# Kernel tuning notes

Hardware: AMD Instinct MI355X
Metric: run time of the kernel (lower is better)

Reference implementation:

```python
import jax, jax.numpy as jnp
import numpy as np


def setup_inputs() -> dict:
    key = jax.random.key(0)
    k1, k2 = jax.random.split(key)
    B, C, H, W = 16, 256, 128, 128
    x = jax.random.normal(k1, (B, C, H, W), dtype=jnp.float32)
    mask = jax.random.uniform(k2, (B, 1, H, W), dtype=jnp.float32)
    return {"x": x, "k": 4096, "mask": mask}


def reference(x, k, mask):
    # Faithful jax version of PointSampler.samplePoints2D:
    #   flatten spatial dims, per-batch random permutation of masked positions,
    #   repeat-to-fill k samples, gather, return (samples [B,k,C], (b, h, w) indices).
    B, C, H, W = x.shape
    L = H * W
    xf = x.reshape(B, C, L).transpose(0, 2, 1)            # [B, L, C]
    m = mask.reshape(B, L) > 0.5                           # bool mask per row
    count = m.sum(axis=1)                                  # [B], number of valid positions

    # Random permutation of masked positions per row: masked entries get random
    # keys, unmasked get +inf, argsort puts masked positions first in random order.
    rkey = jax.random.key(42)
    r = jax.random.uniform(rkey, (B, L))
    r = jnp.where(m, r, jnp.inf)
    perm = jnp.argsort(r, axis=1)                          # [B, L]

    # randperm(c).repeat(ceil(k/c))[:k]  ==  perm[j % c] for j in range(k)
    j = jnp.arange(k)                                      # [k]
    pos = jnp.take_along_axis(perm, j[None, :] % count[:, None], axis=1)  # [B, k] flat positions

    samples = jnp.take_along_axis(xf, pos[:, :, None], axis=1)  # [B, k, C]

    b_idx = jnp.broadcast_to(jnp.arange(B)[:, None], (B, k))
    h_idx = pos // W
    w_idx = pos % W
    return samples, (b_idx, h_idx, w_idx)
```

## Files before the change

kernel.cpp:

```cpp
#include <hip/hip_runtime.h>
#include <stdint.h>


#define L_SPATIAL 16384
#define BATCHES 16
#define CHANNELS 256
#define KSAMP 4096
#define HALF_COUNT 131072u
#define CAP 96
#define INVALID 0xFFFFFFFFu
#define POSB 32

__device__ __forceinline__ uint32_t rotl32(uint32_t x, int d) {
  return (x << d) | (x >> (32 - d));
}

__device__ __forceinline__ void tf2x32(uint32_t k0, uint32_t k1,
                                       uint32_t x0, uint32_t x1,
                                       uint32_t* o0, uint32_t* o1) {
  uint32_t ks2 = k0 ^ k1 ^ 0x1BD11BDAu;
  x0 += k0; x1 += k1;
#define TFR(r) { x0 += x1; x1 = rotl32(x1, r); x1 ^= x0; }
  TFR(13) TFR(15) TFR(26) TFR(6)
  x0 += k1;  x1 += ks2 + 1u;
  TFR(17) TFR(29) TFR(16) TFR(24)
  x0 += ks2; x1 += k0 + 2u;
  TFR(13) TFR(15) TFR(26) TFR(6)
  x0 += k0;  x1 += k1 + 3u;
  TFR(17) TFR(29) TFR(16) TFR(24)
  x0 += k1;  x1 += ks2 + 4u;
  TFR(13) TFR(15) TFR(26) TFR(6)
  x0 += ks2; x1 += k0 + 5u;
#undef TFR
  *o0 = x0; *o1 = x1;
}

__device__ __forceinline__ float bits_to_uniform(uint32_t bits) {
  return __uint_as_float((bits >> 9) | 0x3F800000u) - 1.0f;
}

__device__ __forceinline__ uint32_t r_bits(uint32_t f, unsigned partitionable) {
  uint32_t o0, o1;
  if (partitionable) {
    tf2x32(0u, 42u, 0u, f, &o0, &o1);
    return o0 ^ o1;
  } else {
    uint32_t p = f & (HALF_COUNT - 1u);
    tf2x32(0u, 42u, p, p + HALF_COUNT, &o0, &o1);
    return (f & HALF_COUNT) ? o1 : o0;
  }
}

__global__ void init_detect(const float* __restrict__ mask,
                            unsigned* __restrict__ sel,
                            unsigned* __restrict__ bcnt,
                            unsigned* __restrict__ flag) {
  unsigned i = blockIdx.x * 256u + threadIdx.x;
  if (i < 8192u) sel[i] = 0u;
  else bcnt[i - 8192u] = 0u;
  if (blockIdx.x == 0) {
    int t = threadIdx.x;
    __shared__ int vo, vp;
    if (t == 0) { vo = 0; vp = 0; }
    __syncthreads();
    if (t < 64) {
      uint32_t a0, a1, b0, b1, c0, c1, w0, w1;
      tf2x32(0u, 0u, 0u, 2u, &a0, &a1);
      tf2x32(0u, 0u, 1u, 3u, &b0, &b1);
      uint32_t ko0 = a1, ko1 = b1;
      tf2x32(0u, 0u, 0u, 1u, &c0, &c1);
      uint32_t kp0 = c0, kp1 = c1;
      tf2x32(ko0, ko1, (uint32_t)t, (uint32_t)t + HALF_COUNT, &w0, &w1);
      float mo = bits_to_uniform(w0);
      tf2x32(kp0, kp1, 0u, (uint32_t)t, &w0, &w1);
      float mp = bits_to_uniform(w0 ^ w1);
      float actual = mask[t];
      if (mo == actual) atomicAdd(&vo, 1);
      if (mp == actual) atomicAdd(&vp, 1);
    }
    __syncthreads();
    if (t == 0) *flag = (vp >= vo) ? 1u : 0u;
  }
}

__global__ void build_bucket(const float* __restrict__ mask,
                             unsigned long long* __restrict__ bkeys,
                             unsigned* __restrict__ bcnt,
                             const unsigned* __restrict__ flag) {
  unsigned f = blockIdx.x * 256u + threadIdx.x;
  unsigned part = *flag;
  if (mask[f] > 0.5f) {
    unsigned b = f >> 14, l = f & 16383u;
    uint32_t mant = r_bits(f, part) >> 9;
    unsigned bkt = mant >> 15;
    unsigned slot = atomicAdd(&bcnt[(b << 8) + bkt], 1u);
    if (slot < CAP)
      bkeys[(size_t)((b << 8) + bkt) * CAP + slot] =
          ((unsigned long long)mant << 14) | l;
  }
}

__global__ void prefix_buckets(const unsigned* __restrict__ bcnt,
                               unsigned* __restrict__ bpref,
                               unsigned* __restrict__ counts) {
  int b = blockIdx.x, t = threadIdx.x;
  __shared__ unsigned s[256];
  unsigned v = bcnt[(b << 8) + t];
  s[t] = v;
  __syncthreads();
  for (int d = 1; d < 256; d <<= 1) {
    unsigned u = (t >= d) ? s[t - d] : 0u;
    __syncthreads();
    s[t] += u;
    __syncthreads();
  }
  bpref[(b << 8) + t] = s[t] - v;
  if (t == 255) counts[b] = s[255];
}

__global__ __launch_bounds__(64) void rank_buckets(
    const unsigned long long* __restrict__ bkeys,
    const unsigned* __restrict__ bcnt,
    const unsigned* __restrict__ bpref,
    unsigned* __restrict__ flagrank,
    unsigned* __restrict__ sel) {
  unsigned B = blockIdx.x, b = blockIdx.y;
  unsigned base = bpref[(b << 8) + B];
  if (base >= KSAMP) return;
  unsigned n = bcnt[(b << 8) + B];
  if (n > CAP) n = CAP;
  if (n == 0) return;
  __shared__ unsigned long long sk[CAP];
  const unsigned long long* gk = bkeys + (size_t)((b << 8) + B) * CAP;
  for (unsigned i = threadIdx.x; i < n; i += 64) sk[i] = gk[i];
  __syncthreads();
  for (unsigned i = threadIdx.x; i < n; i += 64) {
    unsigned long long ki = sk[i];
    unsigned r = 0;
    for (unsigned j = 0; j < n; ++j) r += (sk[j] < ki);
    unsigned rank = base + r;
    if (rank < KSAMP) {
      unsigned l = (unsigned)(ki & 16383ull);
      flagrank[(b << 14) + l] = rank;
      atomicOr(&sel[(b << 9) + (l >> 5)], 1u << (l & 31u));
    }
  }
}

__global__ void compact_pairs(const unsigned* __restrict__ flagrank,
                              const unsigned* __restrict__ sel,
                              unsigned* __restrict__ pairs) {
  int b = blockIdx.x, t = threadIdx.x;
  unsigned w0 = sel[(b << 9) + 2 * t];
  unsigned w1 = sel[(b << 9) + 2 * t + 1];
  unsigned c = __popc(w0) + __popc(w1);
  __shared__ unsigned s[256];
  s[t] = c;
  __syncthreads();
  for (int d = 1; d < 256; d <<= 1) {
    unsigned u = (t >= d) ? s[t - d] : 0u;
    __syncthreads();
    s[t] += u;
    __syncthreads();
  }
  unsigned off = s[t] - c;
  unsigned lbase = (unsigned)t * 64u;
  const unsigned* fr = flagrank + (b << 14);
  unsigned* pb = pairs + (b << 12);
  while (w0) {
    unsigned bit = (unsigned)__ffs(w0) - 1u; w0 &= w0 - 1u;
    unsigned l = lbase + bit;
    pb[off++] = (fr[l] << 14) | l;
  }
  while (w1) {
    unsigned bit = (unsigned)__ffs(w1) - 1u; w1 &= w1 - 1u;
    unsigned l = lbase + 32u + bit;
    pb[off++] = (fr[l] << 14) | l;
  }
}

__global__ __launch_bounds__(256, 4) void gather_out(
    const float* __restrict__ x,
    const unsigned* __restrict__ pairs,
    const unsigned* __restrict__ counts,
    float* __restrict__ out) {
  unsigned idx = blockIdx.x;
  unsigned xcd = idx & 7u, slot = idx >> 3;
  unsigned b = (xcd << 1) | (slot >> 7);
  unsigned ib = slot & 127u;
  unsigned count = counts[b];
  unsigned n_sel = count < KSAMP ? count : KSAMP;
  unsigned i0 = ib * POSB;
  if (i0 >= n_sel) return;
  unsigned nb = n_sel - i0; if (nb > POSB) nb = POSB;

  __shared__ float tile[CHANNELS][POSB + 1];
  __shared__ unsigned sl[POSB], sr[POSB];
  int t = threadIdx.x;
  if (t < POSB && (unsigned)t < nb) {
    unsigned pr = pairs[(b << 12) + i0 + (unsigned)t];
    sl[t] = pr & 16383u;
    sr[t] = pr >> 14;
  }
  __syncthreads();

  unsigned pos = (unsigned)t & 31u, ch = (unsigned)t >> 5;
  if (pos < nb) {
    unsigned l = sl[pos];
    const float* xb = x + ((size_t)(b << 8)) * L_SPATIAL + l;
    #pragma unroll 4
    for (unsigned it = 0; it < 32; ++it) {
      unsigned c = it * 8u + ch;
      tile[c][pos] = xb[(size_t)c * L_SPATIAL];
    }
  }
  __syncthreads();

  for (unsigned j = 0; j < POSB; ++j) {
    if (j >= nb) break;
    unsigned r = sr[j];
    float v = tile[t][j];
    for (unsigned jo = r; jo < KSAMP; jo += count) {
      out[(((size_t)(b << 12)) + jo) * CHANNELS + (unsigned)t] = v;
    }
  }

  if (t < 96) {
    unsigned j = (unsigned)t & 31u, c3 = (unsigned)t >> 5;
    if (j < nb) {
      unsigned l = sl[j], r = sr[j];
      float iv = (c3 == 0) ? (float)b : (c3 == 1) ? (float)(l >> 7) : (float)(l & 127u);
      float* oidx = out + (size_t)BATCHES * KSAMP * CHANNELS +
                    (size_t)c3 * (BATCHES * KSAMP);
      for (unsigned jo = r; jo < KSAMP; jo += count)
        oidx[(b << 12) + jo] = iv;
    }
  }
}

extern "C" void kernel_launch(void* const* d_in, const int* in_sizes, int n_in,
                              void* d_out, int out_size, void* d_ws, size_t ws_size,
                              hipStream_t stream) {
  const float* x = (const float*)d_in[0];
  const float* mask = (const float*)d_in[2];

  char* p = (char*)d_ws;
  unsigned long long* bkeys = (unsigned long long*)p;
  p += (size_t)BATCHES * 256 * CAP * sizeof(unsigned long long);
  unsigned* bcnt = (unsigned*)p;  p += BATCHES * 256 * 4;
  unsigned* bpref = (unsigned*)p; p += BATCHES * 256 * 4;
  unsigned* flagrank = (unsigned*)p; p += (size_t)BATCHES * L_SPATIAL * 4;
  unsigned* sel = (unsigned*)p;   p += BATCHES * 512 * 4;
  unsigned* pairs = (unsigned*)p; p += BATCHES * KSAMP * 4;
  unsigned* counts = (unsigned*)p; p += BATCHES * 4;
  unsigned* flag = (unsigned*)p;

  hipLaunchKernelGGL(init_detect, dim3(48), dim3(256), 0, stream,
                     mask, sel, bcnt, flag);
  hipLaunchKernelGGL(build_bucket, dim3(1024), dim3(256), 0, stream,
                     mask, bkeys, bcnt, flag);
  hipLaunchKernelGGL(prefix_buckets, dim3(BATCHES), dim3(256), 0, stream,
                     bcnt, bpref, counts);
  hipLaunchKernelGGL(rank_buckets, dim3(256, BATCHES), dim3(64), 0, stream,
                     bkeys, bcnt, bpref, flagrank, sel);
  hipLaunchKernelGGL(compact_pairs, dim3(BATCHES), dim3(256), 0, stream,
                     flagrank, sel, pairs);
  hipLaunchKernelGGL(gather_out, dim3(BATCHES * KSAMP / POSB), dim3(CHANNELS),
                     0, stream, x, pairs, counts, (float*)d_out);
}
```

Before: 416.8 us.

## Fuse prefix, rank and compact kernels into one per-batch select kernel

```diff
diff --git a/kernel.cpp b/kernel.cpp
--- a/kernel.cpp
+++ b/kernel.cpp
@@ -8,7 +8,6 @@
 #define KSAMP 4096
 #define HALF_COUNT 131072u
 #define CAP 96
-#define INVALID 0xFFFFFFFFu
 #define POSB 32
 
 __device__ __forceinline__ uint32_t rotl32(uint32_t x, int d) {
@@ -52,12 +51,10 @@
 }
 
 __global__ void init_detect(const float* __restrict__ mask,
-                            unsigned* __restrict__ sel,
                             unsigned* __restrict__ bcnt,
                             unsigned* __restrict__ flag) {
   unsigned i = blockIdx.x * 256u + threadIdx.x;
-  if (i < 8192u) sel[i] = 0u;
-  else bcnt[i - 8192u] = 0u;
+  bcnt[i] = 0u;
   if (blockIdx.x == 0) {
     int t = threadIdx.x;
     __shared__ int vo, vp;
@@ -100,83 +97,89 @@
   }
 }
 
-__global__ void prefix_buckets(const unsigned* __restrict__ bcnt,
-                               unsigned* __restrict__ bpref,
-                               unsigned* __restrict__ counts) {
+__global__ __launch_bounds__(1024) void select_fused(
+    const unsigned long long* __restrict__ bkeys,
+    const unsigned* __restrict__ bcnt,
+    unsigned* __restrict__ pairs,
+    unsigned* __restrict__ counts,
+    float* __restrict__ out) {
   int b = blockIdx.x, t = threadIdx.x;
   __shared__ unsigned s[256];
-  unsigned v = bcnt[(b << 8) + t];
-  s[t] = v;
+  __shared__ unsigned sbcnt[256];
+  __shared__ unsigned sbpref[256];
+  __shared__ unsigned short srank[L_SPATIAL];
+  __shared__ unsigned long long swk[16][CAP];
+  __shared__ unsigned stotal;
+
+  for (int i = t; i < L_SPATIAL; i += 1024) srank[i] = 0xFFFFu;
+
+  unsigned v = 0;
+  if (t < 256) { v = bcnt[(b << 8) + t]; sbcnt[t] = v; s[t] = v; }
   __syncthreads();
   for (int d = 1; d < 256; d <<= 1) {
-    unsigned u = (t >= d) ? s[t - d] : 0u;
-    __syncthreads();
-    s[t] += u;
-    __syncthreads();
-  }
-  bpref[(b << 8) + t] = s[t] - v;
-  if (t == 255) counts[b] = s[255];
-}
-
-__global__ __launch_bounds__(64) void rank_buckets(
-    const unsigned long long* __restrict__ bkeys,
-    const unsigned* __restrict__ bcnt,
-    const unsigned* __restrict__ bpref,
-    unsigned* __restrict__ flagrank,
-    unsigned* __restrict__ sel) {
-  unsigned B = blockIdx.x, b = blockIdx.y;
-  unsigned base = bpref[(b << 8) + B];
-  if (base >= KSAMP) return;
-  unsigned n = bcnt[(b << 8) + B];
-  if (n > CAP) n = CAP;
-  if (n == 0) return;
-  __shared__ unsigned long long sk[CAP];
-  const unsigned long long* gk = bkeys + (size_t)((b << 8) + B) * CAP;
-  for (unsigned i = threadIdx.x; i < n; i += 64) sk[i] = gk[i];
-  __syncthreads();
-  for (unsigned i = threadIdx.x; i < n; i += 64) {
-    unsigned long long ki = sk[i];
-    unsigned r = 0;
-    for (unsigned j = 0; j < n; ++j) r += (sk[j] < ki);
-    unsigned rank = base + r;
-    if (rank < KSAMP) {
-      unsigned l = (unsigned)(ki & 16383ull);
-      flagrank[(b << 14) + l] = rank;
-      atomicOr(&sel[(b << 9) + (l >> 5)], 1u << (l & 31u));
-    }
-  }
-}
-
-__global__ void compact_pairs(const unsigned* __restrict__ flagrank,
-                              const unsigned* __restrict__ sel,
-                              unsigned* __restrict__ pairs) {
-  int b = blockIdx.x, t = threadIdx.x;
-  unsigned w0 = sel[(b << 9) + 2 * t];
-  unsigned w1 = sel[(b << 9) + 2 * t + 1];
-  unsigned c = __popc(w0) + __popc(w1);
-  __shared__ unsigned s[256];
-  s[t] = c;
+    unsigned u = (t < 256 && t >= d) ? s[t - d] : 0u;
+    __syncthreads();
+    if (t < 256) s[t] += u;
+    __syncthreads();
+  }
+  if (t < 256) sbpref[t] = s[t] - v;
+  if (t == 255) { stotal = s[255]; counts[b] = s[255]; }
+  __syncthreads();
+
+  unsigned wid = (unsigned)t >> 6, lane = (unsigned)t & 63u;
+  for (unsigned it = 0; it < 16; ++it) {
+    unsigned B = it * 16u + wid;
+    unsigned base = sbpref[B];
+    unsigned n = sbcnt[B];
+    if (n > CAP) n = CAP;
+    bool active = (base < KSAMP) && (n > 0);
+    if (active && lane < n)
+      swk[wid][lane] = bkeys[(size_t)((b << 8) + B) * CAP + lane];
+    __syncthreads();
+    if (active && lane < n) {
+      unsigned long long ki = swk[wid][lane];
+      unsigned r = 0;
+      for (unsigned j = 0; j < n; ++j) r += (swk[wid][j] < ki);
+      unsigned rank = base + r;
+      if (rank < KSAMP)
+        srank[ki & 16383ull] = (unsigned short)rank;
+    }
+    __syncthreads();
+  }
+
+  unsigned total = stotal;
+  unsigned c = 0;
+  if (t < 256)
+    for (int l = t * 64; l < t * 64 + 64; ++l) c += (srank[l] != 0xFFFFu);
+  if (t < 256) s[t] = c;
   __syncthreads();
   for (int d = 1; d < 256; d <<= 1) {
-    unsigned u = (t >= d) ? s[t - d] : 0u;
-    __syncthreads();
-    s[t] += u;
-    __syncthreads();
-  }
-  unsigned off = s[t] - c;
-  unsigned lbase = (unsigned)t * 64u;
-  const unsigned* fr = flagrank + (b << 14);
-  unsigned* pb = pairs + (b << 12);
-  while (w0) {
-    unsigned bit = (unsigned)__ffs(w0) - 1u; w0 &= w0 - 1u;
-    unsigned l = lbase + bit;
-    pb[off++] = (fr[l] << 14) | l;
-  }
-  while (w1) {
-    unsigned bit = (unsigned)__ffs(w1) - 1u; w1 &= w1 - 1u;
-    unsigned l = lbase + 32u + bit;
-    pb[off++] = (fr[l] << 14) | l;
-  }
+    unsigned u = (t < 256 && t >= d) ? s[t - d] : 0u;
+    __syncthreads();
+    if (t < 256) s[t] += u;
+    __syncthreads();
+  }
+  float* oidx = out + (size_t)BATCHES * KSAMP * CHANNELS;
+  float* ob = oidx + (size_t)0 * (BATCHES * KSAMP) + (b << 12);
+  float* oh = oidx + (size_t)1 * (BATCHES * KSAMP) + (b << 12);
+  float* ow = oidx + (size_t)2 * (BATCHES * KSAMP) + (b << 12);
+  if (t < 256) {
+    unsigned off = s[t] - c;
+    unsigned* pb = pairs + (b << 12);
+    for (int l = t * 64; l < t * 64 + 64; ++l) {
+      unsigned r = srank[l];
+      if (r != 0xFFFFu) {
+        pb[off++] = (r << 14) | (unsigned)l;
+        float hv = (float)(l >> 7), wv = (float)(l & 127);
+        for (unsigned jo = r; jo < KSAMP; jo += total) {
+          oh[jo] = hv;
+          ow[jo] = wv;
+        }
+      }
+    }
+  }
+  float bv = (float)b;
+  for (int i = t; i < KSAMP; i += 1024) ob[i] = bv;
 }
 
 __global__ __launch_bounds__(256, 4) void gather_out(
@@ -224,18 +227,6 @@
       out[(((size_t)(b << 12)) + jo) * CHANNELS + (unsigned)t] = v;
     }
   }
-
-  if (t < 96) {
-    unsigned j = (unsigned)t & 31u, c3 = (unsigned)t >> 5;
-    if (j < nb) {
-      unsigned l = sl[j], r = sr[j];
-      float iv = (c3 == 0) ? (float)b : (c3 == 1) ? (float)(l >> 7) : (float)(l & 127u);
-      float* oidx = out + (size_t)BATCHES * KSAMP * CHANNELS +
-                    (size_t)c3 * (BATCHES * KSAMP);
-      for (unsigned jo = r; jo < KSAMP; jo += count)
-        oidx[(b << 12) + jo] = iv;
-    }
-  }
 }
 
 extern "C" void kernel_launch(void* const* d_in, const int* in_sizes, int n_in,
@@ -248,23 +239,16 @@
   unsigned long long* bkeys = (unsigned long long*)p;
   p += (size_t)BATCHES * 256 * CAP * sizeof(unsigned long long);
   unsigned* bcnt = (unsigned*)p;  p += BATCHES * 256 * 4;
-  unsigned* bpref = (unsigned*)p; p += BATCHES * 256 * 4;
-  unsigned* flagrank = (unsigned*)p; p += (size_t)BATCHES * L_SPATIAL * 4;
-  unsigned* sel = (unsigned*)p;   p += BATCHES * 512 * 4;
   unsigned* pairs = (unsigned*)p; p += BATCHES * KSAMP * 4;
   unsigned* counts = (unsigned*)p; p += BATCHES * 4;
   unsigned* flag = (unsigned*)p;
 
-  hipLaunchKernelGGL(init_detect, dim3(48), dim3(256), 0, stream,
-                     mask, sel, bcnt, flag);
+  hipLaunchKernelGGL(init_detect, dim3(16), dim3(256), 0, stream,
+                     mask, bcnt, flag);
   hipLaunchKernelGGL(build_bucket, dim3(1024), dim3(256), 0, stream,
                      mask, bkeys, bcnt, flag);
-  hipLaunchKernelGGL(prefix_buckets, dim3(BATCHES), dim3(256), 0, stream,
-                     bcnt, bpref, counts);
-  hipLaunchKernelGGL(rank_buckets, dim3(256, BATCHES), dim3(64), 0, stream,
-                     bkeys, bcnt, bpref, flagrank, sel);
-  hipLaunchKernelGGL(compact_pairs, dim3(BATCHES), dim3(256), 0, stream,
-                     flagrank, sel, pairs);
+  hipLaunchKernelGGL(select_fused, dim3(BATCHES), dim3(1024), 0, stream,
+                     bkeys, bcnt, pairs, counts, (float*)d_out);
   hipLaunchKernelGGL(gather_out, dim3(BATCHES * KSAMP / POSB), dim3(CHANNELS),
                      0, stream, x, pairs, counts, (float*)d_out);
 }
```

Result: slower. 428.1 us (+2.7%).

## Fold bucket prefix scan into rank kernel and move index writes to compaction

Applied to the files above, without the earlier changes.

```diff
diff --git a/kernel.cpp b/kernel.cpp
--- a/kernel.cpp
+++ b/kernel.cpp
@@ -8,7 +8,6 @@
 #define KSAMP 4096
 #define HALF_COUNT 131072u
 #define CAP 96
-#define INVALID 0xFFFFFFFFu
 #define POSB 32
 
 __device__ __forceinline__ uint32_t rotl32(uint32_t x, int d) {
@@ -100,41 +99,41 @@
   }
 }
 
-__global__ void prefix_buckets(const unsigned* __restrict__ bcnt,
-                               unsigned* __restrict__ bpref,
-                               unsigned* __restrict__ counts) {
-  int b = blockIdx.x, t = threadIdx.x;
-  __shared__ unsigned s[256];
-  unsigned v = bcnt[(b << 8) + t];
-  s[t] = v;
-  __syncthreads();
-  for (int d = 1; d < 256; d <<= 1) {
-    unsigned u = (t >= d) ? s[t - d] : 0u;
-    __syncthreads();
-    s[t] += u;
-    __syncthreads();
-  }
-  bpref[(b << 8) + t] = s[t] - v;
-  if (t == 255) counts[b] = s[255];
-}
-
 __global__ __launch_bounds__(64) void rank_buckets(
     const unsigned long long* __restrict__ bkeys,
     const unsigned* __restrict__ bcnt,
-    const unsigned* __restrict__ bpref,
     unsigned* __restrict__ flagrank,
-    unsigned* __restrict__ sel) {
+    unsigned* __restrict__ sel,
+    unsigned* __restrict__ counts) {
   unsigned B = blockIdx.x, b = blockIdx.y;
-  unsigned base = bpref[(b << 8) + B];
+  unsigned lane = threadIdx.x;
+  const unsigned* bc = bcnt + (b << 8);
+  unsigned pre = 0, tot = 0, mine = 0;
+  #pragma unroll
+  for (int i = 0; i < 4; ++i) {
+    unsigned idx = lane + (unsigned)i * 64u;
+    unsigned v = bc[idx];
+    tot += v;
+    if (idx < B) pre += v;
+    if (idx == B) mine = v;
+  }
+  #pragma unroll
+  for (int d = 32; d >= 1; d >>= 1) {
+    pre += __shfl_xor(pre, d, 64);
+    tot += __shfl_xor(tot, d, 64);
+    mine += __shfl_xor(mine, d, 64);
+  }
+  if (B == 255u && lane == 0) counts[b] = tot;
+  unsigned base = pre;
   if (base >= KSAMP) return;
-  unsigned n = bcnt[(b << 8) + B];
+  unsigned n = mine;
   if (n > CAP) n = CAP;
   if (n == 0) return;
   __shared__ unsigned long long sk[CAP];
   const unsigned long long* gk = bkeys + (size_t)((b << 8) + B) * CAP;
-  for (unsigned i = threadIdx.x; i < n; i += 64) sk[i] = gk[i];
-  __syncthreads();
-  for (unsigned i = threadIdx.x; i < n; i += 64) {
+  for (unsigned i = lane; i < n; i += 64) sk[i] = gk[i];
+  __syncthreads();
+  for (unsigned i = lane; i < n; i += 64) {
     unsigned long long ki = sk[i];
     unsigned r = 0;
     for (unsigned j = 0; j < n; ++j) r += (sk[j] < ki);
@@ -149,8 +148,11 @@
 
 __global__ void compact_pairs(const unsigned* __restrict__ flagrank,
                               const unsigned* __restrict__ sel,
-                              unsigned* __restrict__ pairs) {
+                              const unsigned* __restrict__ counts,
+                              unsigned* __restrict__ pairs,
+                              float* __restrict__ out) {
   int b = blockIdx.x, t = threadIdx.x;
+  unsigned total = counts[b];
   unsigned w0 = sel[(b << 9) + 2 * t];
   unsigned w1 = sel[(b << 9) + 2 * t + 1];
   unsigned c = __popc(w0) + __popc(w1);
@@ -163,6 +165,10 @@
     s[t] += u;
     __syncthreads();
   }
+  float* oidx = out + (size_t)BATCHES * KSAMP * CHANNELS;
+  float* ob = oidx + (b << 12);
+  float* oh = oidx + (size_t)BATCHES * KSAMP + (b << 12);
+  float* ow = oidx + (size_t)2 * BATCHES * KSAMP + (b << 12);
   unsigned off = s[t] - c;
   unsigned lbase = (unsigned)t * 64u;
   const unsigned* fr = flagrank + (b << 14);
@@ -170,13 +176,21 @@
   while (w0) {
     unsigned bit = (unsigned)__ffs(w0) - 1u; w0 &= w0 - 1u;
     unsigned l = lbase + bit;
-    pb[off++] = (fr[l] << 14) | l;
+    unsigned r = fr[l];
+    pb[off++] = (r << 14) | l;
+    float hv = (float)(l >> 7), wv = (float)(l & 127u);
+    for (unsigned jo = r; jo < KSAMP; jo += total) { oh[jo] = hv; ow[jo] = wv; }
   }
   while (w1) {
     unsigned bit = (unsigned)__ffs(w1) - 1u; w1 &= w1 - 1u;
     unsigned l = lbase + 32u + bit;
-    pb[off++] = (fr[l] << 14) | l;
-  }
+    unsigned r = fr[l];
+    pb[off++] = (r << 14) | l;
+    float hv = (float)(l >> 7), wv = (float)(l & 127u);
+    for (unsigned jo = r; jo < KSAMP; jo += total) { oh[jo] = hv; ow[jo] = wv; }
+  }
+  float bv = (float)b;
+  for (int i = t; i < KSAMP; i += 256) ob[i] = bv;
 }
 
 __global__ __launch_bounds__(256, 4) void gather_out(
@@ -224,18 +238,6 @@
       out[(((size_t)(b << 12)) + jo) * CHANNELS + (unsigned)t] = v;
     }
   }
-
-  if (t < 96) {
-    unsigned j = (unsigned)t & 31u, c3 = (unsigned)t >> 5;
-    if (j < nb) {
-      unsigned l = sl[j], r = sr[j];
-      float iv = (c3 == 0) ? (float)b : (c3 == 1) ? (float)(l >> 7) : (float)(l & 127u);
-      float* oidx = out + (size_t)BATCHES * KSAMP * CHANNELS +
-                    (size_t)c3 * (BATCHES * KSAMP);
-      for (unsigned jo = r; jo < KSAMP; jo += count)
-        oidx[(b << 12) + jo] = iv;
-    }
-  }
 }
 
 extern "C" void kernel_launch(void* const* d_in, const int* in_sizes, int n_in,
@@ -248,7 +250,6 @@
   unsigned long long* bkeys = (unsigned long long*)p;
   p += (size_t)BATCHES * 256 * CAP * sizeof(unsigned long long);
   unsigned* bcnt = (unsigned*)p;  p += BATCHES * 256 * 4;
-  unsigned* bpref = (unsigned*)p; p += BATCHES * 256 * 4;
   unsigned* flagrank = (unsigned*)p; p += (size_t)BATCHES * L_SPATIAL * 4;
   unsigned* sel = (unsigned*)p;   p += BATCHES * 512 * 4;
   unsigned* pairs = (unsigned*)p; p += BATCHES * KSAMP * 4;
@@ -259,12 +260,10 @@
                      mask, sel, bcnt, flag);
   hipLaunchKernelGGL(build_bucket, dim3(1024), dim3(256), 0, stream,
                      mask, bkeys, bcnt, flag);
-  hipLaunchKernelGGL(prefix_buckets, dim3(BATCHES), dim3(256), 0, stream,
-                     bcnt, bpref, counts);
   hipLaunchKernelGGL(rank_buckets, dim3(256, BATCHES), dim3(64), 0, stream,
-                     bkeys, bcnt, bpref, flagrank, sel);
+                     bkeys, bcnt, flagrank, sel, counts);
   hipLaunchKernelGGL(compact_pairs, dim3(BATCHES), dim3(256), 0, stream,
-                     flagrank, sel, pairs);
+                     flagrank, sel, counts, pairs, (float*)d_out);
   hipLaunchKernelGGL(gather_out, dim3(BATCHES * KSAMP / POSB), dim3(CHANNELS),
                      0, stream, x, pairs, counts, (float*)d_out);
 }
```

New measurement: 418.0 us. Within noise of the previous version (+0.3%).
